# Kernel tuning notes

Measured on AMD Instinct MI355X. Metric: run time of the kernel, lower is better.

Reference implementation:

```python
import jax, jax.numpy as jnp
import numpy as np

NUM_HEADS = 6
DIM = 192
WS = (2, 6, 12)          # window size (z, h, w)
DATA = (8, 96, 180)      # padded (plev, lat, lon)
SHIFT = (1, 3, 6)


def _position_index(ws):
    Z, H, W = ws
    zi, zj = np.arange(Z), -np.arange(Z) * Z
    hi, hj = np.arange(H), -np.arange(H) * H
    w = np.arange(W)
    c1 = np.stack(np.meshgrid(zi, hi, w, indexing='ij')).reshape(3, -1)
    c2 = np.stack(np.meshgrid(zj, hj, w, indexing='ij')).reshape(3, -1)
    coords = (c1[:, :, None] - c2[:, None, :]).transpose(1, 2, 0).copy()
    coords[:, :, 2] += W - 1
    coords[:, :, 1] *= 2 * W - 1
    coords[:, :, 0] *= (2 * W - 1) * H * H
    return coords.sum(-1).reshape(-1).astype(np.int32)


def _shift_mask(data, ws, ss):
    Z, H, W = data
    img = np.zeros((Z, H, W))
    cnt = 0
    for z in ((0, -ss[0]), (-ss[0], None)):
        for h in ((0, -ss[1]), (-ss[1], None)):
            for w in ((0, None),):  # lam=False: longitude is cyclic, no w split
                img[z[0]:z[1], h[0]:h[1], w[0]:w[1]] = cnt
                cnt += 1
    m = img.reshape(Z // ws[0], ws[0], H // ws[1], ws[1], W // ws[2], ws[2])
    m = m.transpose(0, 2, 4, 1, 3, 5).reshape(-1, ws[0] * ws[1] * ws[2])
    diff = m[:, None, :] - m[:, :, None]
    return np.where(diff != 0, -100.0, 0.0).astype(np.float32)


def setup_inputs() -> dict:
    key = jax.random.key(0)
    ks = jax.random.split(key, 4)
    N = WS[0] * WS[1] * WS[2]                      # 144 tokens / window
    nW = (DATA[0] // WS[0]) * (DATA[1] // WS[1])   # 64 (z,h) window pairs
    wlon = DATA[2] // WS[2]                        # 15 lon windows
    B_ = 1 * nW * wlon                             # 960 total windows (batch=1)
    bias_rows = (2 * WS[2] - 1) * WS[1] ** 2 * WS[0] ** 2  # 3312
    return {
        'x': jax.random.normal(ks[0], (B_, N, DIM), jnp.float32),
        'w1': jax.random.normal(ks[1], (DIM, 3 * DIM), jnp.float32) * 0.02,
        'b1': jnp.zeros((3 * DIM,), jnp.float32),
        'w2': jax.random.normal(ks[2], (DIM, DIM), jnp.float32) * 0.02,
        'b2': jnp.zeros((DIM,), jnp.float32),
        'bias_table': jax.random.normal(ks[3], (bias_rows, nW, NUM_HEADS), jnp.float32) * 0.02,
        'mask': jnp.asarray(_shift_mask(DATA, WS, SHIFT)),
        'position_index': jnp.asarray(_position_index(WS)),
        'batch_size': 1,
    }


def reference(x, w1, b1, w2, b2, bias_table, mask, position_index, batch_size):
    B_, N, C = x.shape
    Ch = C // NUM_HEADS
    scale = Ch ** -0.5
    qkv = (x @ w1 + b1).reshape(B_, N, 3, NUM_HEADS, Ch)
    qkv = jnp.transpose(qkv, (2, 0, 3, 1, 4))      # (3, B_, H, N, Ch)
    q, k, v = qkv[0] * scale, qkv[1], qkv[2]
    attn = jnp.einsum('bhnc,bhmc->bhnm', q, k)      # (B_, H, N, N)
    nW = bias_table.shape[1]
    wlon = B_ // (batch_size * nW)
    # earth-specific bias gather: (N*N,) -> (nW, H, N, N)
    bias = bias_table[position_index].reshape(N, N, nW, NUM_HEADS)
    bias = jnp.transpose(bias, (2, 3, 0, 1))
    attn = attn.reshape(batch_size, nW, wlon, NUM_HEADS, N, N) + bias[None, :, None]
    # shift mask add: (total_windows, N, N) broadcast over batch and heads
    attn = attn.reshape(batch_size, nW * wlon, NUM_HEADS, N, N) + mask[None, :, None]
    attn = jax.nn.softmax(attn.reshape(B_, NUM_HEADS, N, N), axis=-1)
    out = jnp.einsum('bhnm,bhmc->bnhc', attn, v).reshape(B_, N, C)
    return out @ w2 + b2
```

## Files before the change

kernel.cpp:

```cpp
#include <hip/hip_runtime.h>

typedef __attribute__((ext_vector_type(8))) short bf16x8;
typedef __attribute__((ext_vector_type(4))) float f32x4;
typedef unsigned short u16;
typedef unsigned int u32;

#define NTOK 144
#define CDIM 192
#define NH 6
#define CH 32
#define C3 576
#define NWIN 64
#define WLON 15
#define SCALE 0.17677669529663687f
#define LOG2E 1.4426950408889634f

#define OFF_W1T  0u
#define OFF_W2T  221184u
#define OFF_COMB 294912u
#define OFF_Q    16220160u
#define OFF_K    69304320u
#define OFF_V    122388480u

__device__ __forceinline__ u16 f2b(float f){
  u32 u = __float_as_uint(f);
  u32 r = u + 0x7FFFu + ((u >> 16) & 1u);
  return (u16)(r >> 16);
}
__device__ __forceinline__ float b2f(u16 u){
  return __uint_as_float(((u32)u) << 16);
}
__device__ __forceinline__ u32 pk2(float a, float b){
  return (u32)f2b(a) | ((u32)f2b(b) << 16);
}

extern "C" __global__ __launch_bounds__(256) void prep_weights(
    const float* __restrict__ w1, const float* __restrict__ w2,
    u16* __restrict__ w1t, u16* __restrict__ w2t){
  int idx = blockIdx.x * 256 + threadIdx.x;
  if (idx < CDIM * C3){ int k = idx / C3;  int c = idx - k * C3;  w1t[c * CDIM + k] = f2b(w1[idx]); }
  if (idx < CDIM * CDIM){ int k = idx / CDIM; int c = idx - k * CDIM; w2t[c * CDIM + k] = f2b(w2[idx]); }
}

extern "C" __global__ __launch_bounds__(192) void prep_comb(
    const float* __restrict__ bt, const float* __restrict__ mask,
    const int* __restrict__ pidx, u16* __restrict__ comb){
  int nwh = blockIdx.x;
  int nw = nwh / NH, h = nwh - nw * NH;
  int tl = blockIdx.y * 192 + threadIdx.x;
  int ti = tl / 576;
  int rem = tl - ti * 576;
  int nt = rem >> 6, lane = rem & 63;
  int ib = ti * 16 + ((lane >> 4) << 2);
  int j  = nt * 16 + (lane & 15);
  const float* mrow = mask + (size_t)(nw * WLON) * (NTOK * NTOK);
  float v[4];
  #pragma unroll
  for (int r = 0; r < 4; ++r){
    int e = (ib + r) * NTOK + j;
    int pi = pidx[e];
    v[r] = bt[((size_t)pi * NWIN + nw) * NH + h] + mrow[e];
  }
  uint2 out; out.x = pk2(v[0], v[1]); out.y = pk2(v[2], v[3]);
  *reinterpret_cast<uint2*>(comb + ((size_t)nwh * 5184 + tl) * 4) = out;
}

#define BPAD 200
extern "C" __global__ __launch_bounds__(256, 3) void qkv_gemm(
    const float* __restrict__ x, const u16* __restrict__ w1t, const float* __restrict__ b1,
    u16* __restrict__ qw, u16* __restrict__ kw, u16* __restrict__ vw){
  __shared__ u16 Bl[2][64 * BPAD];
  const int tid = threadIdx.x;
  const int wid = tid >> 6, lane = tid & 63, l15 = lane & 15, l4 = lane >> 4;
  const size_t row0 = (size_t)blockIdx.x * 128 + wid * 32;
  const f32x4 zz = {0.f, 0.f, 0.f, 0.f};

  bf16x8 af[2][6];
  #pragma unroll
  for (int mf = 0; mf < 2; ++mf){
    const float* src = x + (row0 + mf * 16 + l15) * CDIM + l4 * 8;
    #pragma unroll
    for (int kk = 0; kk < 6; ++kk){
      float4 f0 = *reinterpret_cast<const float4*>(src + kk * 32);
      float4 f1 = *reinterpret_cast<const float4*>(src + kk * 32 + 4);
      union { bf16x8 v; uint4 u; } cv;
      cv.u.x = pk2(f0.x, f0.y); cv.u.y = pk2(f0.z, f0.w);
      cv.u.z = pk2(f1.x, f1.y); cv.u.w = pk2(f1.z, f1.w);
      af[mf][kk] = cv.v;
    }
  }
  int bw_[2], n0_[2];
  #pragma unroll
  for (int mf = 0; mf < 2; ++mf){
    int t0 = (int)row0 + mf * 16 + l4 * 4;
    bw_[mf] = t0 / NTOK; n0_[mf] = t0 - bw_[mf] * NTOK;
  }

  const int sr = tid >> 2, sq = tid & 3;
  {
    const u16* src = w1t + (size_t)sr * CDIM + sq * 48;
    u16* dst = &Bl[0][sr * BPAD + sq * 48];
    #pragma unroll
    for (int i = 0; i < 48; i += 8)
      *reinterpret_cast<uint4*>(dst + i) = *reinterpret_cast<const uint4*>(src + i);
  }

  int cur = 0;
  #pragma unroll 1
  for (int nt = 0; nt < 9; ++nt){
    __syncthreads();
    if (nt < 8){
      const u16* src = w1t + (size_t)((nt + 1) * 64 + sr) * CDIM + sq * 48;
      u16* dst = &Bl[cur ^ 1][sr * BPAD + sq * 48];
      #pragma unroll
      for (int i = 0; i < 48; i += 8)
        *reinterpret_cast<uint4*>(dst + i) = *reinterpret_cast<const uint4*>(src + i);
    }
    f32x4 acc[2][4];
    #pragma unroll
    for (int mf = 0; mf < 2; ++mf)
      #pragma unroll
      for (int nf = 0; nf < 4; ++nf) acc[mf][nf] = zz;
    #pragma unroll
    for (int kk = 0; kk < 6; ++kk){
      bf16x8 bfr[4];
      #pragma unroll
      for (int nf = 0; nf < 4; ++nf)
        bfr[nf] = *reinterpret_cast<const bf16x8*>(&Bl[cur][(nf * 16 + l15) * BPAD + kk * 32 + l4 * 8]);
      #pragma unroll
      for (int mf = 0; mf < 2; ++mf)
        #pragma unroll
        for (int nf = 0; nf < 4; ++nf)
          acc[mf][nf] = __builtin_amdgcn_mfma_f32_16x16x32_bf16(af[mf][kk], bfr[nf], acc[mf][nf], 0, 0, 0);
    }
    int which = nt / 3;
    #pragma unroll
    for (int nf = 0; nf < 4; ++nf){
      int c = nt * 64 + nf * 16 + l15;
      int rem = c - which * CDIM;
      int hh = rem >> 5, chh = rem & 31;
      float bias = b1[c];
      if (which == 2){
        #pragma unroll
        for (int mf = 0; mf < 2; ++mf){
          uint2 pv;
          pv.x = pk2(acc[mf][nf][0] + bias, acc[mf][nf][1] + bias);
          pv.y = pk2(acc[mf][nf][2] + bias, acc[mf][nf][3] + bias);
          *reinterpret_cast<uint2*>(vw + (((size_t)bw_[mf] * NH + hh) * CH + chh) * NTOK + n0_[mf]) = pv;
        }
      } else {
        u16* base = (which == 0) ? qw : kw;
        float mult = (which == 0) ? SCALE : 1.0f;
        #pragma unroll
        for (int mf = 0; mf < 2; ++mf)
          #pragma unroll
          for (int r = 0; r < 4; ++r)
            base[(((size_t)bw_[mf] * NH + hh) * NTOK + n0_[mf] + r) * CH + chh] = f2b((acc[mf][nf][r] + bias) * mult);
      }
    }
    cur ^= 1;
  }
}

extern "C" __global__ __launch_bounds__(192, 4) void attn_kernel(
    const u16* __restrict__ qw, const u16* __restrict__ kw, const u16* __restrict__ vw,
    const u16* __restrict__ comb, float* __restrict__ outbuf){
  __shared__ u16 Pl[3][16][40];
  const int tid = threadIdx.x;
  const int bh = blockIdx.x;
  const int b = bh / NH, h = bh - b * NH;
  const int wv = tid >> 6, lane = tid & 63, l15 = lane & 15, l4 = lane >> 4;
  const size_t qkbase = ((size_t)b * NH + h) * (NTOK * CH);
  const size_t vbase  = ((size_t)b * NH + h) * (CH * NTOK);
  const size_t cbase  = ((size_t)((b / WLON) * NH + h)) * (5184 * 4);
  u16* Pw = &Pl[wv][0][0];
  u16* stash = reinterpret_cast<u16*>(outbuf);
  const f32x4 zz = {0.f, 0.f, 0.f, 0.f};

  for (int mi = 0; mi < 3; ++mi){
    const int ti = wv * 3 + mi;
    bf16x8 aq = *reinterpret_cast<const bf16x8*>(qw + qkbase + (ti * 16 + l15) * CH + l4 * 8);
    f32x4 s[9];
    #pragma unroll
    for (int nt = 0; nt < 9; ++nt){
      bf16x8 bk = *reinterpret_cast<const bf16x8*>(kw + qkbase + (nt * 16 + l15) * CH + l4 * 8);
      s[nt] = __builtin_amdgcn_mfma_f32_16x16x32_bf16(aq, bk, zz, 0, 0, 0);
    }
    #pragma unroll
    for (int nt = 0; nt < 9; ++nt){
      uint2 cc = *reinterpret_cast<const uint2*>(comb + cbase + ((size_t)(ti * 9 + nt) * 64 + lane) * 4);
      s[nt][0] += b2f((u16)(cc.x & 0xFFFF));
      s[nt][1] += b2f((u16)(cc.x >> 16));
      s[nt][2] += b2f((u16)(cc.y & 0xFFFF));
      s[nt][3] += b2f((u16)(cc.y >> 16));
    }
    float invs[4];
    #pragma unroll
    for (int r = 0; r < 4; ++r){
      float mx = s[0][r];
      #pragma unroll
      for (int nt = 1; nt < 9; ++nt) mx = fmaxf(mx, s[nt][r]);
      #pragma unroll
      for (int off = 8; off; off >>= 1) mx = fmaxf(mx, __shfl_xor(mx, off, 16));
      float sum = 0.f;
      #pragma unroll
      for (int nt = 0; nt < 9; ++nt){
        float p = exp2f((s[nt][r] - mx) * LOG2E);
        s[nt][r] = p; sum += p;
      }
      #pragma unroll
      for (int off = 8; off; off >>= 1) sum += __shfl_xor(sum, off, 16);
      invs[r] = 1.0f / sum;
    }
    f32x4 o0 = zz, o1 = zz;
    #pragma unroll
    for (int kk = 0; kk < 5; ++kk){
      #pragma unroll
      for (int r = 0; r < 4; ++r){
        Pw[(l4 * 4 + r) * 40 + l15] = f2b(s[2 * kk][r]);
        if (kk < 4) Pw[(l4 * 4 + r) * 40 + 16 + l15] = f2b(s[2 * kk + 1][r]);
      }
      int j0 = kk * 32 + l4 * 8;
      int jc = (j0 < NTOK) ? j0 : 0;
      bf16x8 ap = *reinterpret_cast<const bf16x8*>(Pw + l15 * 40 + l4 * 8);
      bf16x8 bv0 = *reinterpret_cast<const bf16x8*>(vw + vbase + (size_t)l15 * NTOK + jc);
      bf16x8 bv1 = *reinterpret_cast<const bf16x8*>(vw + vbase + (size_t)(16 + l15) * NTOK + jc);
      if (j0 >= NTOK) ap = bf16x8{0, 0, 0, 0, 0, 0, 0, 0};
      o0 = __builtin_amdgcn_mfma_f32_16x16x32_bf16(ap, bv0, o0, 0, 0, 0);
      o1 = __builtin_amdgcn_mfma_f32_16x16x32_bf16(ap, bv1, o1, 0, 0, 0);
    }
    #pragma unroll
    for (int r = 0; r < 4; ++r){
      size_t t = (size_t)b * NTOK + ti * 16 + l4 * 4 + r;
      float is = invs[r];
      stash[t * 384 + 192 + h * CH + l15]      = f2b(o0[r] * is);
      stash[t * 384 + 192 + h * CH + 16 + l15] = f2b(o1[r] * is);
    }
  }
}

extern "C" __global__ __launch_bounds__(256, 2) void proj_gemm(
    const u16* __restrict__ w2t, const float* __restrict__ b2, float* __restrict__ outbuf){
  const int tid = threadIdx.x;
  const int wid = tid >> 6, lane = tid & 63, l15 = lane & 15, l4 = lane >> 4;
  const int hb = blockIdx.y;
  const f32x4 zz = {0.f, 0.f, 0.f, 0.f};

  bf16x8 bfr[6][6];
  #pragma unroll
  for (int nf = 0; nf < 6; ++nf)
    #pragma unroll
    for (int kk = 0; kk < 6; ++kk)
      bfr[nf][kk] = *reinterpret_cast<const bf16x8*>(
          w2t + (size_t)(hb * 96 + nf * 16 + l15) * CDIM + kk * 32 + l4 * 8);

  const u16* stash = reinterpret_cast<const u16*>(outbuf);
  const size_t rbase = (size_t)blockIdx.x * 256 + wid * 64;

#define LOADA(dst, mt) { \
    const u16* src_ = stash + (rbase + (mt) * 16 + l15) * 384 + 192 + l4 * 8; \
    _Pragma("unroll") \
    for (int kk = 0; kk < 6; ++kk) dst[kk] = *reinterpret_cast<const bf16x8*>(src_ + kk * 32); }

#define COMPUTE(a_, mt) { \
    f32x4 acc[6]; \
    _Pragma("unroll") \
    for (int nf = 0; nf < 6; ++nf) acc[nf] = zz; \
    _Pragma("unroll") \
    for (int kk = 0; kk < 6; ++kk) \
      _Pragma("unroll") \
      for (int nf = 0; nf < 6; ++nf) \
        acc[nf] = __builtin_amdgcn_mfma_f32_16x16x32_bf16(a_[kk], bfr[nf][kk], acc[nf], 0, 0, 0); \
    _Pragma("unroll") \
    for (int nf = 0; nf < 6; ++nf){ \
      int c = hb * 96 + nf * 16 + l15; \
      float bias = b2[c]; \
      _Pragma("unroll") \
      for (int r = 0; r < 4; ++r) \
        outbuf[(rbase + (mt) * 16 + l4 * 4 + r) * CDIM + c] = acc[nf][r] + bias; } }

  bf16x8 a0[6], a1[6];
  LOADA(a0, 0)
  LOADA(a1, 1) COMPUTE(a0, 0)
  LOADA(a0, 2) COMPUTE(a1, 1)
  LOADA(a1, 3) COMPUTE(a0, 2)
  COMPUTE(a1, 3)
#undef LOADA
#undef COMPUTE
}

extern "C" void kernel_launch(void* const* d_in, const int* in_sizes, int n_in,
                              void* d_out, int out_size, void* d_ws, size_t ws_size,
                              hipStream_t stream){
  const float* x    = (const float*)d_in[0];
  const float* w1   = (const float*)d_in[1];
  const float* b1   = (const float*)d_in[2];
  const float* w2   = (const float*)d_in[3];
  const float* b2   = (const float*)d_in[4];
  const float* bt   = (const float*)d_in[5];
  const float* mask = (const float*)d_in[6];
  const int*   pidx = (const int*)d_in[7];
  (void)in_sizes; (void)n_in; (void)out_size; (void)ws_size;

  char* ws = (char*)d_ws;
  u16* w1t  = (u16*)(ws + OFF_W1T);
  u16* w2t  = (u16*)(ws + OFF_W2T);
  u16* comb = (u16*)(ws + OFF_COMB);
  u16* qw   = (u16*)(ws + OFF_Q);
  u16* kw   = (u16*)(ws + OFF_K);
  u16* vw   = (u16*)(ws + OFF_V);
  float* out = (float*)d_out;

  prep_weights<<<dim3(432), dim3(256), 0, stream>>>(w1, w2, w1t, w2t);
  prep_comb<<<dim3(384, 27), dim3(192), 0, stream>>>(bt, mask, pidx, comb);
  qkv_gemm<<<dim3(1080), dim3(256), 0, stream>>>(x, w1t, b1, qw, kw, vw);
  attn_kernel<<<dim3(5760), dim3(192), 0, stream>>>(qw, kw, vw, comb, out);
  proj_gemm<<<dim3(540, 2), dim3(256), 0, stream>>>(w2t, b2, out);
}
```

Before: 290.5 us.

## Feed fp32 bias+mask as MFMA accumulator, hoist K fragments, drop softmax max

The combined bias+mask table is now stored in fp32 and loaded directly as the MFMA accumulator input, so the separate bf16 unpack-and-add pass disappears. K fragments are loaded once per block and reused across the three query tiles. The row-max subtraction in softmax is removed, on the assumption that scores stay small enough that exp does not overflow. The trade-offs are double the bias-table memory traffic, more registers held for K, and less numerical safety for large logits.

```diff
diff --git a/kernel.cpp b/kernel.cpp
--- a/kernel.cpp
+++ b/kernel.cpp
@@ -18,17 +18,14 @@
 #define OFF_W1T  0u
 #define OFF_W2T  221184u
 #define OFF_COMB 294912u
-#define OFF_Q    16220160u
-#define OFF_K    69304320u
-#define OFF_V    122388480u
+#define OFF_Q    32145408u
+#define OFF_K    85229568u
+#define OFF_V    138313728u
 
 __device__ __forceinline__ u16 f2b(float f){
   u32 u = __float_as_uint(f);
   u32 r = u + 0x7FFFu + ((u >> 16) & 1u);
   return (u16)(r >> 16);
-}
-__device__ __forceinline__ float b2f(u16 u){
-  return __uint_as_float(((u32)u) << 16);
 }
 __device__ __forceinline__ u32 pk2(float a, float b){
   return (u32)f2b(a) | ((u32)f2b(b) << 16);
@@ -44,7 +41,7 @@
 
 extern "C" __global__ __launch_bounds__(192) void prep_comb(
     const float* __restrict__ bt, const float* __restrict__ mask,
-    const int* __restrict__ pidx, u16* __restrict__ comb){
+    const int* __restrict__ pidx, float* __restrict__ comb){
   int nwh = blockIdx.x;
   int nw = nwh / NH, h = nwh - nw * NH;
   int tl = blockIdx.y * 192 + threadIdx.x;
@@ -54,15 +51,15 @@
   int ib = ti * 16 + ((lane >> 4) << 2);
   int j  = nt * 16 + (lane & 15);
   const float* mrow = mask + (size_t)(nw * WLON) * (NTOK * NTOK);
-  float v[4];
+  float4 v;
+  float* vp = reinterpret_cast<float*>(&v);
   #pragma unroll
   for (int r = 0; r < 4; ++r){
     int e = (ib + r) * NTOK + j;
     int pi = pidx[e];
-    v[r] = bt[((size_t)pi * NWIN + nw) * NH + h] + mrow[e];
-  }
-  uint2 out; out.x = pk2(v[0], v[1]); out.y = pk2(v[2], v[3]);
-  *reinterpret_cast<uint2*>(comb + ((size_t)nwh * 5184 + tl) * 4) = out;
+    vp[r] = bt[((size_t)pi * NWIN + nw) * NH + h] + mrow[e];
+  }
+  *reinterpret_cast<float4*>(comb + ((size_t)nwh * 5184 + tl) * 4) = v;
 }
 
 #define BPAD 200
@@ -164,7 +161,7 @@
 
 extern "C" __global__ __launch_bounds__(192, 4) void attn_kernel(
     const u16* __restrict__ qw, const u16* __restrict__ kw, const u16* __restrict__ vw,
-    const u16* __restrict__ comb, float* __restrict__ outbuf){
+    const float* __restrict__ comb, float* __restrict__ outbuf){
   __shared__ u16 Pl[3][16][40];
   const int tid = threadIdx.x;
   const int bh = blockIdx.x;
@@ -172,40 +169,33 @@
   const int wv = tid >> 6, lane = tid & 63, l15 = lane & 15, l4 = lane >> 4;
   const size_t qkbase = ((size_t)b * NH + h) * (NTOK * CH);
   const size_t vbase  = ((size_t)b * NH + h) * (CH * NTOK);
-  const size_t cbase  = ((size_t)((b / WLON) * NH + h)) * (5184 * 4);
+  const float* cb = comb + ((size_t)((b / WLON) * NH + h)) * (5184 * 4);
   u16* Pw = &Pl[wv][0][0];
   u16* stash = reinterpret_cast<u16*>(outbuf);
   const f32x4 zz = {0.f, 0.f, 0.f, 0.f};
 
+  bf16x8 bk[9];
+  #pragma unroll
+  for (int nt = 0; nt < 9; ++nt)
+    bk[nt] = *reinterpret_cast<const bf16x8*>(kw + qkbase + (nt * 16 + l15) * CH + l4 * 8);
+
+  #pragma unroll 1
   for (int mi = 0; mi < 3; ++mi){
     const int ti = wv * 3 + mi;
     bf16x8 aq = *reinterpret_cast<const bf16x8*>(qw + qkbase + (ti * 16 + l15) * CH + l4 * 8);
     f32x4 s[9];
     #pragma unroll
     for (int nt = 0; nt < 9; ++nt){
-      bf16x8 bk = *reinterpret_cast<const bf16x8*>(kw + qkbase + (nt * 16 + l15) * CH + l4 * 8);
-      s[nt] = __builtin_amdgcn_mfma_f32_16x16x32_bf16(aq, bk, zz, 0, 0, 0);
-    }
-    #pragma unroll
-    for (int nt = 0; nt < 9; ++nt){
-      uint2 cc = *reinterpret_cast<const uint2*>(comb + cbase + ((size_t)(ti * 9 + nt) * 64 + lane) * 4);
-      s[nt][0] += b2f((u16)(cc.x & 0xFFFF));
-      s[nt][1] += b2f((u16)(cc.x >> 16));
-      s[nt][2] += b2f((u16)(cc.y & 0xFFFF));
-      s[nt][3] += b2f((u16)(cc.y >> 16));
+      f32x4 cf = *reinterpret_cast<const f32x4*>(cb + ((size_t)(ti * 9 + nt) * 64 + lane) * 4);
+      s[nt] = __builtin_amdgcn_mfma_f32_16x16x32_bf16(aq, bk[nt], cf, 0, 0, 0);
     }
     float invs[4];
     #pragma unroll
     for (int r = 0; r < 4; ++r){
-      float mx = s[0][r];
-      #pragma unroll
-      for (int nt = 1; nt < 9; ++nt) mx = fmaxf(mx, s[nt][r]);
-      #pragma unroll
-      for (int off = 8; off; off >>= 1) mx = fmaxf(mx, __shfl_xor(mx, off, 16));
       float sum = 0.f;
       #pragma unroll
       for (int nt = 0; nt < 9; ++nt){
-        float p = exp2f((s[nt][r] - mx) * LOG2E);
+        float p = exp2f(s[nt][r] * LOG2E);
         s[nt][r] = p; sum += p;
       }
       #pragma unroll
@@ -303,12 +293,12 @@
   (void)in_sizes; (void)n_in; (void)out_size; (void)ws_size;
 
   char* ws = (char*)d_ws;
-  u16* w1t  = (u16*)(ws + OFF_W1T);
-  u16* w2t  = (u16*)(ws + OFF_W2T);
-  u16* comb = (u16*)(ws + OFF_COMB);
-  u16* qw   = (u16*)(ws + OFF_Q);
-  u16* kw   = (u16*)(ws + OFF_K);
-  u16* vw   = (u16*)(ws + OFF_V);
+  u16*   w1t  = (u16*)(ws + OFF_W1T);
+  u16*   w2t  = (u16*)(ws + OFF_W2T);
+  float* comb = (float*)(ws + OFF_COMB);
+  u16*   qw   = (u16*)(ws + OFF_Q);
+  u16*   kw   = (u16*)(ws + OFF_K);
+  u16*   vw   = (u16*)(ws + OFF_V);
   float* out = (float*)d_out;
 
   prep_weights<<<dim3(432), dim3(256), 0, stream>>>(w1, w2, w1t, w2t);
```

Result: no change. 292.5 us (+0.7%).
